# Performance work log

Hardware: AMD Instinct MI355X
Metric: run time of the kernel (lower is better)

The kernel has to match this reference:

```python
import jax, jax.numpy as jnp
import numpy as np
from jax import lax

# db2 (Daubechies-2) filter bank, identical to pywt.Wavelet('db2')
_s3 = np.sqrt(3.0)
_dn = 4.0 * np.sqrt(2.0)
_h = np.array([(1 + _s3) / _dn, (3 + _s3) / _dn, (3 - _s3) / _dn, (1 - _s3) / _dn], dtype=np.float32)  # h0..h3
DEC_LO = jnp.asarray(_h[::-1].copy())                                                # [h3,h2,h1,h0]
DEC_HI = jnp.asarray(np.array([-_h[0], _h[1], -_h[2], _h[3]], dtype=np.float32))
REC_LO = jnp.asarray(_h)                                                             # [h0,h1,h2,h3]
REC_HI = jnp.asarray(np.array([_h[3], -_h[2], _h[1], -_h[0]], dtype=np.float32))
FL = 4  # filter length


def dwt1_symmetric(x):
    """pywt.wavedec level-1, mode='symmetric' along axis 1. x: [B,S,H] -> (cA,cD) each [B,(S+3)//2,H]."""
    B, S, H = x.shape
    M = (S + FL - 1) // 2
    xe = jnp.pad(x, ((0, 0), (FL - 1, FL - 1), (0, 0)), mode='symmetric')  # [B,S+6,H]

    def corr(w):
        # a[k] = sum_t w[FL-1-t] * xe[2k+1+t]
        return sum(w[FL - 1 - t] * xe[:, 1 + t:1 + t + 2 * M:2, :] for t in range(FL))

    return corr(DEC_LO), corr(DEC_HI)


def idwt1(ca, cd):
    """pywt.waverec level-1 (idwt). ca,cd: [B,Mc,H] -> [B,2*Mc-FL+2,H]."""
    B, Mc, H = ca.shape
    up_len = 2 * Mc - 1
    out_len = 2 * Mc - FL + 2

    def branch(c, f):
        u = jnp.zeros((B, up_len + 4, H), dtype=c.dtype)  # zero pad FL-2=2 each side
        u = u.at[:, 2:2 + up_len:2, :].set(c)             # upsample (zeros at odd positions)
        return sum(f[j] * u[:, 4 - j:4 - j + out_len, :] for j in range(FL))

    return branch(ca, REC_LO) + branch(cd, REC_HI)


def conv3_same(c, w, b):
    """torch Conv1d(H,H,3,padding=1) on channel-last c: [B,T,H]; w: [Hout,Hin,3], b: [Hout]."""
    y = lax.conv_general_dilated(c.transpose(0, 2, 1), w, window_strides=(1,),
                                 padding=((1, 1),), dimension_numbers=('NCH', 'OIH', 'NCH'))
    return (y + b[None, :, None]).transpose(0, 2, 1)


def setup_inputs() -> dict:
    key = jax.random.key(0)
    ks = jax.random.split(key, 7)
    B, S, H = 8, 2048, 1024
    sc_conv = 1.0 / np.sqrt(3 * H)
    sc_lin = 1.0 / np.sqrt(H)
    return {
        'x': jax.random.normal(ks[0], (B, S, H), jnp.float32),
        'w_approx': jax.random.normal(ks[1], (H, H, 3), jnp.float32) * sc_conv,
        'b_approx': jax.random.normal(ks[2], (H,), jnp.float32) * 0.01,
        'w_detail': jax.random.normal(ks[3], (H, H, 3), jnp.float32) * sc_conv,
        'b_detail': jax.random.normal(ks[4], (H,), jnp.float32) * 0.01,
        'w_out': jax.random.normal(ks[5], (H, H), jnp.float32) * sc_lin,
        'b_out': jax.random.normal(ks[6], (H,), jnp.float32) * 0.01,
    }


def reference(x, w_approx, b_approx, w_detail, b_detail, w_out, b_out):
    B, S, H = x.shape
    if S % 2 != 0:  # static pad to even length (matches torch code)
        x = jnp.pad(x, ((0, 0), (0, 1), (0, 0)))
        S += 1
    ca, cd = dwt1_symmetric(x)          # [B, S//2+1, H]
    target = S // 2
    ca, cd = ca[:, :target, :], cd[:, :target, :]  # truncate like the torch module
    pa = jax.nn.gelu(conv3_same(ca, w_approx, b_approx), approximate=False)
    pd = jax.nn.gelu(conv3_same(cd, w_detail, b_detail), approximate=False)
    recon = idwt1(pa, pd)               # [B, S-2, H]
    recon = jnp.pad(recon, ((0, 0), (0, S - recon.shape[1]), (0, 0)))  # zero-pad to S
    out = jnp.einsum('bsh,oh->bso', recon, w_out) + b_out  # output_proj; dropout=identity (eval)
    return out
```

## Files before the change

kernel.cpp:

```cpp
#include <hip/hip_runtime.h>
#include <hip/hip_bf16.h>
#include <math.h>


namespace {

constexpr int Hc = 1024;
constexpr int Sc = 2048;
constexpr int Mcv = 1024;
constexpr int AROWS = 1026;

constexpr double S3d = 1.7320508075688772935274463;
constexpr double DNd = 5.6568542494923801952067549;
constexpr float W0 = (float)((1.0 + S3d) / DNd);
constexpr float W1 = (float)((3.0 + S3d) / DNd);
constexpr float W2 = (float)((3.0 - S3d) / DNd);
constexpr float W3 = (float)((1.0 - S3d) / DNd);

typedef short bf16x8 __attribute__((ext_vector_type(8)));
typedef float f32x4 __attribute__((ext_vector_type(4)));

typedef __attribute__((address_space(1))) const unsigned char ga_u8;
typedef __attribute__((address_space(3))) unsigned char la_u8;

__device__ __forceinline__ void gload16(const void* g, void* l) {
  __builtin_amdgcn_global_load_lds((ga_u8*)g, (la_u8*)l, 16, 0, 0);
}

__device__ __forceinline__ unsigned short rnd1(float v) {
  __hip_bfloat16 hb = __float2bfloat16(v);
  return *reinterpret_cast<unsigned short*>(&hb);
}

__device__ __forceinline__ ushort4 rnd4(const float4 v) {
  ushort4 h;
  h.x = rnd1(v.x); h.y = rnd1(v.y); h.z = rnd1(v.z); h.w = rnd1(v.w);
  return h;
}

__device__ __forceinline__ void split1(float v, unsigned short& h, unsigned short& l) {
  __hip_bfloat16 hb = __float2bfloat16(v);
  float r = v - __bfloat162float(hb);
  __hip_bfloat16 lb = __float2bfloat16(r);
  h = *reinterpret_cast<unsigned short*>(&hb);
  l = *reinterpret_cast<unsigned short*>(&lb);
}

__device__ __forceinline__ void split4(const float4 v, ushort4& h, ushort4& l) {
  split1(v.x, h.x, l.x);
  split1(v.y, h.y, l.y);
  split1(v.z, h.z, l.z);
  split1(v.w, h.w, l.w);
}

__global__ void dwt_kernel(const float* __restrict__ x,
                           unsigned short* __restrict__ A) {
  const int tid = blockIdx.x * 256 + threadIdx.x;
  const int h4 = (tid & 255) << 2;
  const int mp = (tid >> 8) & 511;
  const int b = tid >> 17;
  const int m = mp * 2;
  const float* xb = x + (size_t)b * Sc * Hc;
  float4 v[6];
#pragma unroll
  for (int t = 0; t < 6; ++t) {
    int i = 2 * m - 2 + t;
    if (i < 0) i = -i - 1;
    v[t] = *reinterpret_cast<const float4*>(&xb[(size_t)i * Hc + h4]);
  }
  float4 a0, d0, a1, d1;
#define DWT_AD(ao, dd, u0, u1, u2, u3)                      \
  ao.x = W0*u0.x + W1*u1.x + W2*u2.x + W3*u3.x;             \
  ao.y = W0*u0.y + W1*u1.y + W2*u2.y + W3*u3.y;             \
  ao.z = W0*u0.z + W1*u1.z + W2*u2.z + W3*u3.z;             \
  ao.w = W0*u0.w + W1*u1.w + W2*u2.w + W3*u3.w;             \
  dd.x = W3*u0.x - W2*u1.x + W1*u2.x - W0*u3.x;             \
  dd.y = W3*u0.y - W2*u1.y + W1*u2.y - W0*u3.y;             \
  dd.z = W3*u0.z - W2*u1.z + W1*u2.z - W0*u3.z;             \
  dd.w = W3*u0.w - W2*u1.w + W1*u2.w - W0*u3.w;
  DWT_AD(a0, d0, v[0], v[1], v[2], v[3]);
  DWT_AD(a1, d1, v[2], v[3], v[4], v[5]);
#undef DWT_AD

  const size_t rowA = (size_t)b * AROWS + 1 + m;
  const size_t rowD = (size_t)(b + 8) * AROWS + 1 + m;
  *reinterpret_cast<ushort4*>(&A[rowA * Hc + h4]) = rnd4(a0);
  *reinterpret_cast<ushort4*>(&A[(rowA + 1) * Hc + h4]) = rnd4(a1);
  *reinterpret_cast<ushort4*>(&A[rowD * Hc + h4]) = rnd4(d0);
  *reinterpret_cast<ushort4*>(&A[(rowD + 1) * Hc + h4]) = rnd4(d1);

  if (mp == 0) {
    const ushort4 z4 = {0, 0, 0, 0};
    const size_t gr[4] = {(size_t)b * AROWS,       (size_t)b * AROWS + AROWS - 1,
                          (size_t)(b + 8) * AROWS, (size_t)(b + 8) * AROWS + AROWS - 1};
#pragma unroll
    for (int i = 0; i < 4; ++i)
      *reinterpret_cast<ushort4*>(&A[gr[i] * Hc + h4]) = z4;
  }
}

__global__ void prep_conv_w(const float* __restrict__ wA, const float* __restrict__ wD,
                            unsigned short* __restrict__ aH, unsigned short* __restrict__ aL,
                            unsigned short* __restrict__ dH, unsigned short* __restrict__ dL) {
  const int idx = blockIdx.x * 256 + threadIdx.x;
  const int i4 = idx & 255;
  const int o = (idx >> 8) & 1023;
  const int c = idx >> 18;
  const float* w = c ? wD : wA;
  unsigned short* oh = c ? dH : aH;
  unsigned short* ol = c ? dL : aL;
  const float* src = w + (size_t)o * 3072 + i4 * 12;
  const float4 f0 = *reinterpret_cast<const float4*>(src);
  const float4 f1 = *reinterpret_cast<const float4*>(src + 4);
  const float4 f2 = *reinterpret_cast<const float4*>(src + 8);
  const float e[12] = {f0.x, f0.y, f0.z, f0.w, f1.x, f1.y, f1.z, f1.w,
                       f2.x, f2.y, f2.z, f2.w};
#pragma unroll
  for (int k = 0; k < 3; ++k) {
    float4 v = make_float4(e[k], e[3 + k], e[6 + k], e[9 + k]);
    ushort4 hh, ll;
    split4(v, hh, ll);
    const size_t off = (size_t)k * 1048576 + (size_t)o * 1024 + i4 * 4;
    *reinterpret_cast<ushort4*>(&oh[off]) = hh;
    *reinterpret_cast<ushort4*>(&ol[off]) = ll;
  }
}

__global__ void prep_wout(const float* __restrict__ w,
                          unsigned short* __restrict__ oh, unsigned short* __restrict__ ol) {
  const int idx = blockIdx.x * 256 + threadIdx.x;
  const size_t off = (size_t)(idx >> 8) * 1024 + (idx & 255) * 4;
  ushort4 hh, ll;
  split4(*reinterpret_cast<const float4*>(&w[off]), hh, ll);
  *reinterpret_cast<ushort4*>(&oh[off]) = hh;
  *reinterpret_cast<ushort4*>(&ol[off]) = ll;
}

__global__ __launch_bounds__(512, 2) void conv_mm_kernel(
    const unsigned short* __restrict__ A,
    const unsigned short* __restrict__ BAh, const unsigned short* __restrict__ BAl,
    const unsigned short* __restrict__ BDh, const unsigned short* __restrict__ BDl,
    const float* __restrict__ biasA, const float* __restrict__ biasD,
    float* __restrict__ Yout) {
  __shared__ __align__(16) unsigned short lds[65664];

  const int tid = threadIdx.x;
  const int lane = tid & 63;
  const int wave = tid >> 6;
  const int wm = wave >> 2;
  const int wn = wave & 3;

  const int id = blockIdx.x;
  const int t = id & 3;
  const int o = (id >> 2) & 7;
  const int z = id >> 5;
  const int o0 = o * 128;
  const int t0 = t * 256;
  const int arow0 = z * AROWS + t0;

  const unsigned short* BH = (z < 8) ? BAh : BDh;
  const unsigned short* BL = (z < 8) ? BAl : BDl;
  const float* bias = (z < 8) ? biasA : biasD;

  f32x4 acc[8][2];
#pragma unroll
  for (int m = 0; m < 8; ++m)
#pragma unroll
    for (int n = 0; n < 2; ++n) acc[m][n] = (f32x4){0.f, 0.f, 0.f, 0.f};

  const int q = lane >> 2;
  const int srcslot = (lane & 3) ^ ((lane >> 3) & 3);
  const int l15 = lane & 15;
  const int g = lane >> 4;

#define CONV_STAGE(buf, c0)                                                     \
  {                                                                             \
    unsigned short* L = lds + (buf) * 32832;                                    \
    _Pragma("unroll")                                                           \
    for (int j = 0; j < 2; ++j) {                                               \
      const int seg = wave * 2 + j;                                             \
      const int r = seg * 16 + q;                                               \
      gload16(A + (size_t)(arow0 + r) * 1024 + (c0) + srcslot * 8,              \
              L + seg * 512);                                                   \
    }                                                                           \
    if (wave == 0 && lane < 8) {                                                \
      const int r = 256 + (lane >> 2);                                          \
      gload16(A + (size_t)(arow0 + r) * 1024 + (c0) + (lane & 3) * 8,           \
              L + 8192);                                                        \
    }                                                                           \
    _Pragma("unroll")                                                           \
    for (int j = 0; j < 6; ++j) {                                               \
      const int g6 = wave * 6 + j;                                              \
      const int tp = g6 >> 3;                                                   \
      const int seg = g6 & 7;                                                   \
      const unsigned short* bp =                                                \
          ((tp & 1) ? BL : BH) + (size_t)(tp >> 1) * 1048576;                   \
      const int r = seg * 16 + q;                                               \
      gload16(bp + (size_t)(o0 + r) * 1024 + (c0) + srcslot * 8,                \
              L + 8256 + tp * 4096 + seg * 512);                                \
    }                                                                           \
  }

  CONV_STAGE(0, 0);
  __syncthreads();

  int cur = 0;
#pragma unroll 1
  for (int step = 0; step < 32; ++step) {
    if (step < 31) CONV_STAGE(cur ^ 1, (step + 1) * 32);

    unsigned short* L = lds + cur * 32832;
#pragma unroll
    for (int tap = 0; tap < 3; ++tap) {
      bf16x8 a4[8];
#pragma unroll
      for (int m = 0; m < 8; ++m) {
        const int r = wm * 128 + m * 16 + l15 + tap;
        a4[m] = *reinterpret_cast<const bf16x8*>(L + r * 32 + (g ^ ((r >> 1) & 3)) * 8);
      }
#pragma unroll
      for (int n = 0; n < 2; ++n) {
        const int r = wn * 32 + n * 16 + l15;
        const int off = r * 32 + (g ^ ((r >> 1) & 3)) * 8;
        const bf16x8 bH4 = *reinterpret_cast<const bf16x8*>(L + 8256 + (tap * 2) * 4096 + off);
        const bf16x8 bL4 = *reinterpret_cast<const bf16x8*>(L + 8256 + (tap * 2 + 1) * 4096 + off);
#pragma unroll
        for (int m = 0; m < 8; ++m) {
          acc[m][n] = __builtin_amdgcn_mfma_f32_16x16x32_bf16(a4[m], bH4, acc[m][n], 0, 0, 0);
          acc[m][n] = __builtin_amdgcn_mfma_f32_16x16x32_bf16(a4[m], bL4, acc[m][n], 0, 0, 0);
        }
      }
    }
    __syncthreads();
    cur ^= 1;
  }
#undef CONV_STAGE

  const int yrow0 = z * Mcv + t0 + wm * 128;
  constexpr float RS2 = 0.70710678118654752440f;
#pragma unroll
  for (int n = 0; n < 2; ++n) {
    const int col = o0 + wn * 32 + n * 16 + l15;
    const float bv = bias[col];
#pragma unroll
    for (int m = 0; m < 8; ++m) {
      const int rbase = yrow0 + m * 16 + g * 4;
#pragma unroll
      for (int r = 0; r < 4; ++r) {
        float v = acc[m][n][r] + bv;
        v = 0.5f * v * (1.f + erff(v * RS2));
        Yout[(size_t)(rbase + r) * 1024 + col] = v;
      }
    }
  }
}

__global__ void idwt_kernel(const float* __restrict__ pout,
                            unsigned short* __restrict__ rc) {
  const int tid = blockIdx.x * 256 + threadIdx.x;
  const int h4 = (tid & 255) << 2;
  const int j = (tid >> 8) & 1023;
  const int b = tid >> 18;
  const size_t ro = ((size_t)b * Sc + 2 * j) * Hc + h4;
  if (j == 1023) {
    const ushort4 z4 = {0, 0, 0, 0};
    *reinterpret_cast<ushort4*>(&rc[ro]) = z4;
    *reinterpret_cast<ushort4*>(&rc[ro + Hc]) = z4;
    return;
  }
  const float* pab = pout + (size_t)b * Mcv * Hc;
  const float* pdb = pout + (size_t)(b + 8) * Mcv * Hc;
  const float4 aL = *reinterpret_cast<const float4*>(&pab[(size_t)j * Hc + h4]);
  const float4 aH = *reinterpret_cast<const float4*>(&pab[(size_t)(j + 1) * Hc + h4]);
  const float4 dL = *reinterpret_cast<const float4*>(&pdb[(size_t)j * Hc + h4]);
  const float4 dH = *reinterpret_cast<const float4*>(&pdb[(size_t)(j + 1) * Hc + h4]);
  float4 r0, r1;
  r0.x = W0 * aH.x + W2 * aL.x + W3 * dH.x + W1 * dL.x;
  r0.y = W0 * aH.y + W2 * aL.y + W3 * dH.y + W1 * dL.y;
  r0.z = W0 * aH.z + W2 * aL.z + W3 * dH.z + W1 * dL.z;
  r0.w = W0 * aH.w + W2 * aL.w + W3 * dH.w + W1 * dL.w;
  r1.x = W1 * aH.x + W3 * aL.x - W2 * dH.x - W0 * dL.x;
  r1.y = W1 * aH.y + W3 * aL.y - W2 * dH.y - W0 * dL.y;
  r1.z = W1 * aH.z + W3 * aL.z - W2 * dH.z - W0 * dL.z;
  r1.w = W1 * aH.w + W3 * aL.w - W2 * dH.w - W0 * dL.w;
  *reinterpret_cast<ushort4*>(&rc[ro]) = rnd4(r0);
  *reinterpret_cast<ushort4*>(&rc[ro + Hc]) = rnd4(r1);
}

__global__ __launch_bounds__(256, 2) void gemm_out_kernel(
    const unsigned short* __restrict__ Arc,
    const unsigned short* __restrict__ Bhi, const unsigned short* __restrict__ Blo,
    const float* __restrict__ bias, float* __restrict__ out) {
  __shared__ __align__(16) unsigned short lds[32768];

  const int tid = threadIdx.x;
  const int lane = tid & 63;
  const int wave = tid >> 6;
  const int wm = wave >> 1, wn = wave & 1;

  const int id = blockIdx.x;
  const int rowt = (id >> 6) * 8 + (id & 7);
  const int col = (id >> 3) & 7;
  const int o0 = col * 128;
  const int t0 = rowt * 256;

  f32x4 acc[8][4];
#pragma unroll
  for (int m = 0; m < 8; ++m)
#pragma unroll
    for (int n = 0; n < 4; ++n) acc[m][n] = (f32x4){0.f, 0.f, 0.f, 0.f};

  const int q = lane >> 2;
  const int srcslot = (lane & 3) ^ ((lane >> 3) & 3);
  const int l15 = lane & 15;
  const int g = lane >> 4;

#define GEMM_STAGE(buf, c0)                                                     \
  {                                                                             \
    unsigned short* L = lds + (buf) * 16384;                                    \
    _Pragma("unroll")                                                           \
    for (int j = 0; j < 4; ++j) {                                               \
      const int seg = wave * 4 + j;                                             \
      const int r = seg * 16 + q;                                               \
      gload16(Arc + (size_t)(t0 + r) * 1024 + (c0) + srcslot * 8,               \
              L + seg * 512);                                                   \
    }                                                                           \
    _Pragma("unroll")                                                           \
    for (int j = 0; j < 4; ++j) {                                               \
      const int g4 = wave * 4 + j;                                              \
      const int pl = g4 >> 3;                                                   \
      const int seg = g4 & 7;                                                   \
      const unsigned short* bp = pl ? Blo : Bhi;                                \
      const int r = seg * 16 + q;                                               \
      gload16(bp + (size_t)(o0 + r) * 1024 + (c0) + srcslot * 8,                \
              L + 8192 + pl * 4096 + seg * 512);                                \
    }                                                                           \
  }

  GEMM_STAGE(0, 0);
  __syncthreads();

  int cur = 0;
#pragma unroll 1
  for (int step = 0; step < 32; ++step) {
    if (step < 31) GEMM_STAGE(cur ^ 1, (step + 1) * 32);

    unsigned short* L = lds + cur * 16384;
    bf16x8 a4[8], bH4[4], bL4[4];
#pragma unroll
    for (int m = 0; m < 8; ++m) {
      const int r = wm * 128 + m * 16 + l15;
      a4[m] = *reinterpret_cast<const bf16x8*>(L + r * 32 + (g ^ ((r >> 1) & 3)) * 8);
    }
#pragma unroll
    for (int n = 0; n < 4; ++n) {
      const int r = wn * 64 + n * 16 + l15;
      const int off = r * 32 + (g ^ ((r >> 1) & 3)) * 8;
      bH4[n] = *reinterpret_cast<const bf16x8*>(L + 8192 + off);
      bL4[n] = *reinterpret_cast<const bf16x8*>(L + 12288 + off);
    }
#pragma unroll
    for (int m = 0; m < 8; ++m)
#pragma unroll
      for (int n = 0; n < 4; ++n) {
        acc[m][n] = __builtin_amdgcn_mfma_f32_16x16x32_bf16(a4[m], bH4[n], acc[m][n], 0, 0, 0);
        acc[m][n] = __builtin_amdgcn_mfma_f32_16x16x32_bf16(a4[m], bL4[n], acc[m][n], 0, 0, 0);
      }
    __syncthreads();
    cur ^= 1;
  }
#undef GEMM_STAGE

  const int yrow0 = t0 + wm * 128;
#pragma unroll
  for (int n = 0; n < 4; ++n) {
    const int colg = o0 + wn * 64 + n * 16 + l15;
    const float bv = bias[colg];
#pragma unroll
    for (int m = 0; m < 8; ++m) {
      const int rbase = yrow0 + m * 16 + g * 4;
#pragma unroll
      for (int r = 0; r < 4; ++r)
        out[(size_t)(rbase + r) * 1024 + colg] = acc[m][n][r] + bv;
    }
  }
}

}

extern "C" void kernel_launch(void* const* d_in, const int* in_sizes, int n_in,
                              void* d_out, int out_size, void* d_ws, size_t ws_size,
                              hipStream_t stream) {
  const float* x = (const float*)d_in[0];
  const float* w_approx = (const float*)d_in[1];
  const float* b_approx = (const float*)d_in[2];
  const float* w_detail = (const float*)d_in[3];
  const float* b_detail = (const float*)d_in[4];
  const float* w_out = (const float*)d_in[5];
  const float* b_out = (const float*)d_in[6];
  float* out = (float*)d_out;

  char* ws = (char*)d_ws;
  unsigned short* A = (unsigned short*)(ws);
  float* pout = (float*)(ws + 33619968);
  unsigned short* rc = (unsigned short*)(ws + 100728832);
  unsigned short* wtAh = (unsigned short*)(ws + 134348800);
  unsigned short* wtAl = (unsigned short*)(ws + 140640256);
  unsigned short* wtDh = (unsigned short*)(ws + 146931712);
  unsigned short* wtDl = (unsigned short*)(ws + 153223168);
  unsigned short* woH = (unsigned short*)(ws + 159514624);
  unsigned short* woL = (unsigned short*)(ws + 161611776);

  prep_conv_w<<<2048, 256, 0, stream>>>(w_approx, w_detail, wtAh, wtAl, wtDh, wtDl);
  prep_wout<<<1024, 256, 0, stream>>>(w_out, woH, woL);
  dwt_kernel<<<4096, 256, 0, stream>>>(x, A);

  conv_mm_kernel<<<512, 512, 0, stream>>>(A, wtAh, wtAl, wtDh, wtDl,
                                          b_approx, b_detail, pout);

  idwt_kernel<<<8192, 256, 0, stream>>>(pout, rc);

  gemm_out_kernel<<<512, 256, 0, stream>>>(rc, woH, woL, b_out, out);
}
```

Measured before the change: 408.9 us.

## Store conv GELU output as bf16 and enlarge output GEMM tile to 256x256

```diff
diff --git a/kernel.cpp b/kernel.cpp
--- a/kernel.cpp
+++ b/kernel.cpp
@@ -18,6 +18,7 @@
 constexpr float W3 = (float)((1.0 - S3d) / DNd);
 
 typedef short bf16x8 __attribute__((ext_vector_type(8)));
+typedef unsigned short u16x8 __attribute__((ext_vector_type(8)));
 typedef float f32x4 __attribute__((ext_vector_type(4)));
 
 typedef __attribute__((address_space(1))) const unsigned char ga_u8;
@@ -30,6 +31,12 @@
 __device__ __forceinline__ unsigned short rnd1(float v) {
   __hip_bfloat16 hb = __float2bfloat16(v);
   return *reinterpret_cast<unsigned short*>(&hb);
+}
+
+__device__ __forceinline__ float b2f(unsigned short s) {
+  union { unsigned int u; float f; } c;
+  c.u = ((unsigned int)s) << 16;
+  return c.f;
 }
 
 __device__ __forceinline__ ushort4 rnd4(const float4 v) {
@@ -141,7 +148,7 @@
     const unsigned short* __restrict__ BAh, const unsigned short* __restrict__ BAl,
     const unsigned short* __restrict__ BDh, const unsigned short* __restrict__ BDl,
     const float* __restrict__ biasA, const float* __restrict__ biasD,
-    float* __restrict__ Yout) {
+    unsigned short* __restrict__ Yout) {
   __shared__ __align__(16) unsigned short lds[65664];
 
   const int tid = threadIdx.x;
@@ -249,59 +256,60 @@
       for (int r = 0; r < 4; ++r) {
         float v = acc[m][n][r] + bv;
         v = 0.5f * v * (1.f + erff(v * RS2));
-        Yout[(size_t)(rbase + r) * 1024 + col] = v;
+        Yout[(size_t)(rbase + r) * 1024 + col] = rnd1(v);
       }
     }
   }
 }
 
-__global__ void idwt_kernel(const float* __restrict__ pout,
+__global__ void idwt_kernel(const unsigned short* __restrict__ pout,
                             unsigned short* __restrict__ rc) {
   const int tid = blockIdx.x * 256 + threadIdx.x;
-  const int h4 = (tid & 255) << 2;
-  const int j = (tid >> 8) & 1023;
-  const int b = tid >> 18;
-  const size_t ro = ((size_t)b * Sc + 2 * j) * Hc + h4;
+  const int h8 = (tid & 127) << 3;
+  const int j = (tid >> 7) & 1023;
+  const int b = tid >> 17;
+  const size_t ro = ((size_t)b * Sc + 2 * j) * Hc + h8;
   if (j == 1023) {
-    const ushort4 z4 = {0, 0, 0, 0};
-    *reinterpret_cast<ushort4*>(&rc[ro]) = z4;
-    *reinterpret_cast<ushort4*>(&rc[ro + Hc]) = z4;
+    const u16x8 z8 = {0, 0, 0, 0, 0, 0, 0, 0};
+    *reinterpret_cast<u16x8*>(&rc[ro]) = z8;
+    *reinterpret_cast<u16x8*>(&rc[ro + Hc]) = z8;
     return;
   }
-  const float* pab = pout + (size_t)b * Mcv * Hc;
-  const float* pdb = pout + (size_t)(b + 8) * Mcv * Hc;
-  const float4 aL = *reinterpret_cast<const float4*>(&pab[(size_t)j * Hc + h4]);
-  const float4 aH = *reinterpret_cast<const float4*>(&pab[(size_t)(j + 1) * Hc + h4]);
-  const float4 dL = *reinterpret_cast<const float4*>(&pdb[(size_t)j * Hc + h4]);
-  const float4 dH = *reinterpret_cast<const float4*>(&pdb[(size_t)(j + 1) * Hc + h4]);
-  float4 r0, r1;
-  r0.x = W0 * aH.x + W2 * aL.x + W3 * dH.x + W1 * dL.x;
-  r0.y = W0 * aH.y + W2 * aL.y + W3 * dH.y + W1 * dL.y;
-  r0.z = W0 * aH.z + W2 * aL.z + W3 * dH.z + W1 * dL.z;
-  r0.w = W0 * aH.w + W2 * aL.w + W3 * dH.w + W1 * dL.w;
-  r1.x = W1 * aH.x + W3 * aL.x - W2 * dH.x - W0 * dL.x;
-  r1.y = W1 * aH.y + W3 * aL.y - W2 * dH.y - W0 * dL.y;
-  r1.z = W1 * aH.z + W3 * aL.z - W2 * dH.z - W0 * dL.z;
-  r1.w = W1 * aH.w + W3 * aL.w - W2 * dH.w - W0 * dL.w;
-  *reinterpret_cast<ushort4*>(&rc[ro]) = rnd4(r0);
-  *reinterpret_cast<ushort4*>(&rc[ro + Hc]) = rnd4(r1);
-}
-
-__global__ __launch_bounds__(256, 2) void gemm_out_kernel(
+  const unsigned short* pab = pout + (size_t)b * Mcv * Hc;
+  const unsigned short* pdb = pout + (size_t)(b + 8) * Mcv * Hc;
+  const u16x8 aL = *reinterpret_cast<const u16x8*>(&pab[(size_t)j * Hc + h8]);
+  const u16x8 aH = *reinterpret_cast<const u16x8*>(&pab[(size_t)(j + 1) * Hc + h8]);
+  const u16x8 dL = *reinterpret_cast<const u16x8*>(&pdb[(size_t)j * Hc + h8]);
+  const u16x8 dH = *reinterpret_cast<const u16x8*>(&pdb[(size_t)(j + 1) * Hc + h8]);
+  u16x8 r0, r1;
+#pragma unroll
+  for (int e = 0; e < 8; ++e) {
+    const float faL = b2f(aL[e]), faH = b2f(aH[e]);
+    const float fdL = b2f(dL[e]), fdH = b2f(dH[e]);
+    r0[e] = rnd1(W0 * faH + W2 * faL + W3 * fdH + W1 * fdL);
+    r1[e] = rnd1(W1 * faH + W3 * faL - W2 * fdH - W0 * fdL);
+  }
+  *reinterpret_cast<u16x8*>(&rc[ro]) = r0;
+  *reinterpret_cast<u16x8*>(&rc[ro + Hc]) = r1;
+}
+
+__global__ __launch_bounds__(512, 2) void gemm_out_kernel(
     const unsigned short* __restrict__ Arc,
     const unsigned short* __restrict__ Bhi, const unsigned short* __restrict__ Blo,
     const float* __restrict__ bias, float* __restrict__ out) {
-  __shared__ __align__(16) unsigned short lds[32768];
+  __shared__ __align__(16) unsigned short lds[49152];
 
   const int tid = threadIdx.x;
   const int lane = tid & 63;
   const int wave = tid >> 6;
-  const int wm = wave >> 1, wn = wave & 1;
+  const int wm = wave >> 2;
+  const int wn = wave & 3;
 
   const int id = blockIdx.x;
-  const int rowt = (id >> 6) * 8 + (id & 7);
-  const int col = (id >> 3) & 7;
-  const int o0 = col * 128;
+  const int wgid = (id & 7) * 32 + (id >> 3);
+  const int rowt = wgid >> 2;
+  const int colt = wgid & 3;
+  const int o0 = colt * 256;
   const int t0 = rowt * 256;
 
   f32x4 acc[8][4];
@@ -317,10 +325,10 @@
 
 #define GEMM_STAGE(buf, c0)                                                     \
   {                                                                             \
-    unsigned short* L = lds + (buf) * 16384;                                    \
+    unsigned short* L = lds + (buf) * 24576;                                    \
     _Pragma("unroll")                                                           \
-    for (int j = 0; j < 4; ++j) {                                               \
-      const int seg = wave * 4 + j;                                             \
+    for (int j = 0; j < 2; ++j) {                                               \
+      const int seg = wave * 2 + j;                                             \
       const int r = seg * 16 + q;                                               \
       gload16(Arc + (size_t)(t0 + r) * 1024 + (c0) + srcslot * 8,               \
               L + seg * 512);                                                   \
@@ -328,12 +336,12 @@
     _Pragma("unroll")                                                           \
     for (int j = 0; j < 4; ++j) {                                               \
       const int g4 = wave * 4 + j;                                              \
-      const int pl = g4 >> 3;                                                   \
-      const int seg = g4 & 7;                                                   \
+      const int pl = g4 >> 4;                                                   \
+      const int seg = g4 & 15;                                                  \
       const unsigned short* bp = pl ? Blo : Bhi;                                \
       const int r = seg * 16 + q;                                               \
       gload16(bp + (size_t)(o0 + r) * 1024 + (c0) + srcslot * 8,                \
-              L + 8192 + pl * 4096 + seg * 512);                                \
+              L + 8192 + pl * 8192 + seg * 512);                                \
     }                                                                           \
   }
 
@@ -345,7 +353,7 @@
   for (int step = 0; step < 32; ++step) {
     if (step < 31) GEMM_STAGE(cur ^ 1, (step + 1) * 32);
 
-    unsigned short* L = lds + cur * 16384;
+    unsigned short* L = lds + cur * 24576;
     bf16x8 a4[8], bH4[4], bL4[4];
 #pragma unroll
     for (int m = 0; m < 8; ++m) {
@@ -357,7 +365,7 @@
       const int r = wn * 64 + n * 16 + l15;
       const int off = r * 32 + (g ^ ((r >> 1) & 3)) * 8;
       bH4[n] = *reinterpret_cast<const bf16x8*>(L + 8192 + off);
-      bL4[n] = *reinterpret_cast<const bf16x8*>(L + 12288 + off);
+      bL4[n] = *reinterpret_cast<const bf16x8*>(L + 16384 + off);
     }
 #pragma unroll
     for (int m = 0; m < 8; ++m)
@@ -402,8 +410,8 @@
 
   char* ws = (char*)d_ws;
   unsigned short* A = (unsigned short*)(ws);
-  float* pout = (float*)(ws + 33619968);
-  unsigned short* rc = (unsigned short*)(ws + 100728832);
+  unsigned short* pout = (unsigned short*)(ws + 33619968);
+  unsigned short* rc = (unsigned short*)(ws + 67174400);
   unsigned short* wtAh = (unsigned short*)(ws + 134348800);
   unsigned short* wtAl = (unsigned short*)(ws + 140640256);
   unsigned short* wtDh = (unsigned short*)(ws + 146931712);
@@ -418,7 +426,7 @@
   conv_mm_kernel<<<512, 512, 0, stream>>>(A, wtAh, wtAl, wtDh, wtDl,
                                           b_approx, b_detail, pout);
 
-  idwt_kernel<<<8192, 256, 0, stream>>>(pout, rc);
-
-  gemm_out_kernel<<<512, 256, 0, stream>>>(rc, woH, woL, b_out, out);
-}
+  idwt_kernel<<<4096, 256, 0, stream>>>(pout, rc);
+
+  gemm_out_kernel<<<256, 512, 0, stream>>>(rc, woH, woL, b_out, out);
+}
```

Result: faster. 384.7 us (-5.9%).
